# Performance work log

Measured on AMD Instinct MI355X. Metric: run time of the kernel, lower is better.

Reference implementation:

```python
import jax, jax.numpy as jnp
from jax import lax
import numpy as np

B, T, I, H, OUT = 4096, 168, 4, 64, 12


def setup_inputs() -> dict:
    key = jax.random.key(0)
    ks = jax.random.split(key, 14)
    s = 0.05
    return {
        "x": jax.random.normal(ks[0], (B, T, I), dtype=jnp.float32),
        # LSTM layer 0 (PyTorch gate order: i, f, g, o)
        "Wih0": jax.random.normal(ks[1], (4 * H, I), dtype=jnp.float32) * s,
        "Whh0": jax.random.normal(ks[2], (4 * H, H), dtype=jnp.float32) * s,
        "bih0": jax.random.normal(ks[3], (4 * H,), dtype=jnp.float32) * s,
        "bhh0": jax.random.normal(ks[4], (4 * H,), dtype=jnp.float32) * s,
        # LSTM layer 1
        "Wih1": jax.random.normal(ks[5], (4 * H, H), dtype=jnp.float32) * s,
        "Whh1": jax.random.normal(ks[6], (4 * H, H), dtype=jnp.float32) * s,
        "bih1": jax.random.normal(ks[7], (4 * H,), dtype=jnp.float32) * s,
        "bhh1": jax.random.normal(ks[8], (4 * H,), dtype=jnp.float32) * s,
        # FC head: Linear(64,64) -> ReLU -> Linear(64,12)
        "W1": jax.random.normal(ks[9], (64, H), dtype=jnp.float32) * s,
        "b1": jax.random.normal(ks[10], (64,), dtype=jnp.float32) * s,
        "W2": jax.random.normal(ks[11], (OUT, 64), dtype=jnp.float32) * s,
        "b2": jax.random.normal(ks[12], (OUT,), dtype=jnp.float32) * s,
    }


def _lstm_layer(x, Wih, Whh, bih, bhh):
    # x: [B, T, in]; returns hidden sequence [B, T, H]
    Bsz = x.shape[0]
    Hd = Whh.shape[1]
    # Precompute input contribution for all timesteps: [B, T, 4H]
    xg = jnp.einsum('bti,gi->btg', x, Wih) + bih + bhh

    def step(carry, xg_t):
        h, c = carry
        g = xg_t + h @ Whh.T  # [B, 4H]
        i, f, gg, o = jnp.split(g, 4, axis=-1)
        i = jax.nn.sigmoid(i)
        f = jax.nn.sigmoid(f)
        gg = jnp.tanh(gg)
        o = jax.nn.sigmoid(o)
        c = f * c + i * gg
        h = o * jnp.tanh(c)
        return (h, c), h

    h0 = jnp.zeros((Bsz, Hd), x.dtype)
    (_, _), hs = lax.scan(step, (h0, h0), jnp.swapaxes(xg, 0, 1))  # hs: [T, B, H]
    return jnp.swapaxes(hs, 0, 1)


def reference(x, Wih0, Whh0, bih0, bhh0, Wih1, Whh1, bih1, bhh1, W1, b1, W2, b2):
    # Eval-mode forward: dropout layers are identity.
    h1 = _lstm_layer(x, Wih0, Whh0, bih0, bhh0)   # [B, T, H]
    h2 = _lstm_layer(h1, Wih1, Whh1, bih1, bhh1)  # [B, T, H]
    last = h2[:, -1, :]                            # [B, H]
    z = jax.nn.relu(last @ W1.T + b1)              # [B, 64]
    out = z @ W2.T + b2                            # [B, 12]
    return out.reshape(-1, 3, 4)
```

## Files before the change

kernel.cpp:

```cpp
#include <hip/hip_runtime.h>


typedef _Float16 h8 __attribute__((ext_vector_type(8)));
typedef _Float16 h4 __attribute__((ext_vector_type(4)));
typedef float f4 __attribute__((ext_vector_type(4)));

#define ROWB 208
#define HBUF (16 * ROWB)
#define XTAB_OFF 0
#define XTAB_BYTES (169 * 256)
#define H0_OFF XTAB_BYTES
#define H1_OFF (H0_OFF + 2 * HBUF)
#define SMEM_TOTAL (H1_OFF + 2 * HBUF)

#define K1F 1.4426950408889634f
#define K2F 2.8853900817779268f

__device__ __forceinline__ float exp2_(float x) {
#if __has_builtin(__builtin_amdgcn_exp2f)
  return __builtin_amdgcn_exp2f(x);
#else
  float r; asm("v_exp_f32 %0, %1" : "=v"(r) : "v"(x)); return r;
#endif
}
__device__ __forceinline__ float rcp_(float x) {
#if __has_builtin(__builtin_amdgcn_rcpf)
  return __builtin_amdgcn_rcpf(x);
#else
  float r; asm("v_rcp_f32 %0, %1" : "=v"(r) : "v"(x)); return r;
#endif
}

__device__ __forceinline__ f4 mfma16(h8 a, h8 b, f4 c) {
  return __builtin_amdgcn_mfma_f32_16x16x32_f16(a, b, c, 0, 0, 0);
}

__device__ __forceinline__ h8 load_w8s(const float* __restrict__ p, float sc) {
  h8 r;
#pragma unroll
  for (int j = 0; j < 8; j++) r[j] = (_Float16)(p[j] * sc);
  return r;
}

__device__ __forceinline__ unsigned packh2(float a, float b) {
  unsigned lo = (unsigned)__builtin_bit_cast(unsigned short, (_Float16)a);
  unsigned hi = (unsigned)__builtin_bit_cast(unsigned short, (_Float16)b);
  return lo | (hi << 16);
}

__device__ __forceinline__ void lstm_act(f4 a, float& c, float& h) {
  float Ei = exp2_(-a[0]);
  float Ef = exp2_(-a[1]);
  float Eg = exp2_(a[2]);
  float Eo = exp2_(-a[3]);
  float A = 1.f + Ei, B = 1.f + Ef, C = 1.f + Eg, D = 1.f + Eo;
  float AB = A * B, CD = C * D, BD = B * D;
  float R  = rcp_(AB * CD);
  float fv = (A * CD) * R;
  float ig = (BD * (Eg - 1.f)) * R;
  float ov = (AB * C) * R;
  c = fv * c + ig;
  float r2 = rcp_(exp2_(c * K2F) + 1.f);
  h = ov * (1.f - 2.f * r2);
}

extern "C" __global__ void __launch_bounds__(256, 1)
weather_lstm_mfma6(const float* __restrict__ x,
                   const float* __restrict__ Wih0, const float* __restrict__ Whh0,
                   const float* __restrict__ bih0, const float* __restrict__ bhh0,
                   const float* __restrict__ Wih1, const float* __restrict__ Whh1,
                   const float* __restrict__ bih1, const float* __restrict__ bhh1,
                   const float* __restrict__ W1, const float* __restrict__ b1,
                   const float* __restrict__ W2, const float* __restrict__ b2,
                   float* __restrict__ out)
{
  __shared__ __align__(16) unsigned char smem[SMEM_TOTAL];
  const int tid  = threadIdx.x;
  const int lane = tid & 63;
  const int w    = tid >> 6;
  const int col  = lane & 15;
  const int quad = lane >> 4;
  const int sB   = blockIdx.x * 16;
  const int ub   = w * 16;

  const int g_  = col & 3;
  const int ul_ = col >> 2;
  const float asc = (g_ == 2) ? K2F : K1F;

  h8 a0[4][3], a1i[4][2], a1h[4][2];
#pragma unroll
  for (int T = 0; T < 4; T++) {
    const int unit = ub + (T >> 1) * 8 + 2 * ul_ + (T & 1);
    const int r = g_ * 64 + unit;
#pragma unroll
    for (int f = 0; f < 2; f++) {
      a0[T][f]  = load_w8s(Whh0 + r * 64 + f * 32 + quad * 8, asc);
      a1i[T][f] = load_w8s(Wih1 + r * 64 + f * 32 + quad * 8, asc);
      a1h[T][f] = load_w8s(Whh1 + r * 64 + f * 32 + quad * 8, asc);
    }
    h8 xw = {};
    if (quad == 0) {
#pragma unroll
      for (int j = 0; j < 4; j++) xw[j] = (_Float16)(Wih0[r * 4 + j] * asc);
    }
    a0[T][2] = xw;
  }

  f4 bias0v[4], bias1v[4];
#pragma unroll
  for (int T = 0; T < 4; T++) {
#pragma unroll
    for (int reg = 0; reg < 4; reg++) {
      const int rr = reg * 64 + ub + (T >> 1) * 8 + 2 * quad + (T & 1);
      const float bs = (reg == 2) ? K2F : K1F;
      bias0v[T][reg] = (bih0[rr] + bhh0[rr]) * bs;
      bias1v[T][reg] = (bih1[rr] + bhh1[rr]) * bs;
    }
  }

  for (int idx = tid; idx < SMEM_TOTAL / 4; idx += 256) ((int*)smem)[idx] = 0;
  __syncthreads();
  for (int idx = tid; idx < 16 * 168; idx += 256) {
    const int c_ = idx / 168, t_ = idx - c_ * 168;
    f4 xv = *(const f4*)(x + ((size_t)(sB + c_) * 168 + t_) * 4);
    h4 xh;
#pragma unroll
    for (int j = 0; j < 4; j++) xh[j] = (_Float16)xv[j];
    *(h4*)(smem + XTAB_OFF + t_ * 256 + c_ * 16) = xh;
  }
  __syncthreads();

  float c0[4] = {0.f, 0.f, 0.f, 0.f}, c1[4] = {0.f, 0.f, 0.f, 0.f};
  float hl[4] = {0.f, 0.f, 0.f, 0.f};
  const int bo  = col * ROWB + quad * 16;
  const int wo0 = col * ROWB + (ub + 2 * quad) * 2;
  const int wo1 = wo0 + 16;
  const unsigned char* xp = smem + XTAB_OFF + col * 16;

  for (int k = 0; k <= 168; k++) {
    const int kb = k & 1, kbn = kb ^ 1;
    const unsigned char* h0r = smem + H0_OFF + kbn * HBUF;
    unsigned char*       h0w = smem + H0_OFF + kb  * HBUF;
    const unsigned char* h1r = smem + H1_OFF + kb  * HBUF;
    unsigned char*       h1w = smem + H1_OFF + kbn * HBUF;

    h8 b0  = *(const h8*)(h0r + bo);
    h8 b1v = *(const h8*)(h0r + bo + 64);
    h8 bx  = *(const h8*)(xp + k * 256);
    h8 q0  = *(const h8*)(h1r + bo);
    h8 q1  = *(const h8*)(h1r + bo + 64);

    f4 A[4], C[4];
#pragma unroll
    for (int T = 0; T < 4; T++) A[T] = mfma16(a0[T][0], b0, bias0v[T]);
#pragma unroll
    for (int T = 0; T < 4; T++) C[T] = mfma16(a1i[T][0], b0, bias1v[T]);
#pragma unroll
    for (int T = 0; T < 4; T++) A[T] = mfma16(a0[T][1], b1v, A[T]);
#pragma unroll
    for (int T = 0; T < 4; T++) C[T] = mfma16(a1i[T][1], b1v, C[T]);
#pragma unroll
    for (int T = 0; T < 4; T++) A[T] = mfma16(a0[T][2], bx, A[T]);
#pragma unroll
    for (int T = 0; T < 4; T++) C[T] = mfma16(a1h[T][0], q0, C[T]);
#pragma unroll
    for (int T = 0; T < 4; T++) C[T] = mfma16(a1h[T][1], q1, C[T]);

    if (k < 168) {
      float h0o[4];
#pragma unroll
      for (int T = 0; T < 4; T++) lstm_act(A[T], c0[T], h0o[T]);
      *(unsigned*)(h0w + wo0) = packh2(h0o[0], h0o[1]);
      *(unsigned*)(h0w + wo1) = packh2(h0o[2], h0o[3]);
    }
    if (k > 0) {
#pragma unroll
      for (int T = 0; T < 4; T++) lstm_act(C[T], c1[T], hl[T]);
      *(unsigned*)(h1w + wo0) = packh2(hl[0], hl[1]);
      *(unsigned*)(h1w + wo1) = packh2(hl[2], hl[3]);
    }
    __syncthreads();
  }

  float* fh = (float*)smem;
#pragma unroll
  for (int T = 0; T < 4; T++)
    fh[col * 64 + (ub + (T >> 1) * 8 + 2 * quad + (T & 1))] = hl[T];
  __syncthreads();

  {
    const int u = tid & 63, grp = tid >> 6;
    float za[4];
#pragma unroll
    for (int i = 0; i < 4; i++) za[i] = b1[u];
    const float* w1r = W1 + u * 64;
    for (int j = 0; j < 64; j++) {
      float wv = w1r[j];
#pragma unroll
      for (int i = 0; i < 4; i++) za[i] += wv * fh[(grp * 4 + i) * 64 + j];
    }
    float* zl = (float*)(smem + 4096);
#pragma unroll
    for (int i = 0; i < 4; i++)
      zl[(grp * 4 + i) * 64 + u] = fmaxf(za[i], 0.f);
  }
  __syncthreads();

  if (tid < 192) {
    const float* zl = (const float*)(smem + 4096);
    const int s = tid / 12, o = tid - s * 12;
    float a = b2[o];
    for (int j = 0; j < 64; j++) a += W2[o * 64 + j] * zl[s * 64 + j];
    out[(sB + s) * 12 + o] = a;
  }
}

extern "C" void kernel_launch(void* const* d_in, const int* in_sizes, int n_in,
                              void* d_out, int out_size, void* d_ws, size_t ws_size,
                              hipStream_t stream) {
  (void)in_sizes; (void)n_in; (void)d_ws; (void)ws_size; (void)out_size;
  const float* x    = (const float*)d_in[0];
  const float* Wih0 = (const float*)d_in[1];
  const float* Whh0 = (const float*)d_in[2];
  const float* bih0 = (const float*)d_in[3];
  const float* bhh0 = (const float*)d_in[4];
  const float* Wih1 = (const float*)d_in[5];
  const float* Whh1 = (const float*)d_in[6];
  const float* bih1 = (const float*)d_in[7];
  const float* bhh1 = (const float*)d_in[8];
  const float* W1   = (const float*)d_in[9];
  const float* b1   = (const float*)d_in[10];
  const float* W2   = (const float*)d_in[11];
  const float* b2   = (const float*)d_in[12];

  weather_lstm_mfma6<<<dim3(256), dim3(256), 0, stream>>>(
      x, Wih0, Whh0, bih0, bhh0, Wih1, Whh1, bih1, bhh1, W1, b1, W2, b2,
      (float*)d_out);
}
```

Before: 234.7 us.

## Split LSTM layers onto separate warp groups with counter-based LDS handoff

Doubles the block to 512 threads. Four waves run layer 0 and four waves run layer 1, and they talk through a four-slot ring of layer-0 hidden states instead of meeting at a block-wide barrier on every step. Workgroup-scope atomic counters with acquire/release spin loops replace __syncthreads, so layer 0 can run up to a few steps ahead of layer 1 and each wave keeps fewer weight registers. The cost is busy-wait spinning on LDS counters and more waves per block. Memory ordering between the layer-0 writes and the counter increment rests on a single lane's release atomic, which is a correctness risk.

```diff
diff --git a/kernel.cpp b/kernel.cpp
--- a/kernel.cpp
+++ b/kernel.cpp
@@ -8,10 +8,11 @@
 #define ROWB 208
 #define HBUF (16 * ROWB)
 #define XTAB_OFF 0
-#define XTAB_BYTES (169 * 256)
+#define XTAB_BYTES (168 * 256)
 #define H0_OFF XTAB_BYTES
-#define H1_OFF (H0_OFF + 2 * HBUF)
-#define SMEM_TOTAL (H1_OFF + 2 * HBUF)
+#define H1_OFF (H0_OFF + 4 * HBUF)
+#define CNT_OFF (H1_OFF + 2 * HBUF)
+#define SMEM_TOTAL (CNT_OFF + 128)
 
 #define K1F 1.4426950408889634f
 #define K2F 2.8853900817779268f
@@ -59,13 +60,21 @@
   float fv = (A * CD) * R;
   float ig = (BD * (Eg - 1.f)) * R;
   float ov = (AB * C) * R;
-  c = fv * c + ig;
+  c = fmaf(fv, c, ig);
   float r2 = rcp_(exp2_(c * K2F) + 1.f);
-  h = ov * (1.f - 2.f * r2);
-}
-
-extern "C" __global__ void __launch_bounds__(256, 1)
-weather_lstm_mfma6(const float* __restrict__ x,
+  h = ov * fmaf(-2.f, r2, 1.f);
+}
+
+__device__ __forceinline__ void spin_ge(int* p, int tgt) {
+  while (__hip_atomic_load(p, __ATOMIC_ACQUIRE, __HIP_MEMORY_SCOPE_WORKGROUP) < tgt) {}
+}
+__device__ __forceinline__ void arrive(int* p, int lane) {
+  if (lane == 0)
+    __hip_atomic_fetch_add(p, 1, __ATOMIC_RELEASE, __HIP_MEMORY_SCOPE_WORKGROUP);
+}
+
+extern "C" __global__ void __launch_bounds__(512, 2)
+weather_lstm_mfma8(const float* __restrict__ x,
                    const float* __restrict__ Wih0, const float* __restrict__ Whh0,
                    const float* __restrict__ bih0, const float* __restrict__ bhh0,
                    const float* __restrict__ Wih1, const float* __restrict__ Whh1,
@@ -81,46 +90,20 @@
   const int col  = lane & 15;
   const int quad = lane >> 4;
   const int sB   = blockIdx.x * 16;
-  const int ub   = w * 16;
+  const bool isA = (w < 4);
+  const int gw   = w & 3;
+  const int ub   = gw * 16;
 
   const int g_  = col & 3;
   const int ul_ = col >> 2;
   const float asc = (g_ == 2) ? K2F : K1F;
 
-  h8 a0[4][3], a1i[4][2], a1h[4][2];
-#pragma unroll
-  for (int T = 0; T < 4; T++) {
-    const int unit = ub + (T >> 1) * 8 + 2 * ul_ + (T & 1);
-    const int r = g_ * 64 + unit;
-#pragma unroll
-    for (int f = 0; f < 2; f++) {
-      a0[T][f]  = load_w8s(Whh0 + r * 64 + f * 32 + quad * 8, asc);
-      a1i[T][f] = load_w8s(Wih1 + r * 64 + f * 32 + quad * 8, asc);
-      a1h[T][f] = load_w8s(Whh1 + r * 64 + f * 32 + quad * 8, asc);
-    }
-    h8 xw = {};
-    if (quad == 0) {
-#pragma unroll
-      for (int j = 0; j < 4; j++) xw[j] = (_Float16)(Wih0[r * 4 + j] * asc);
-    }
-    a0[T][2] = xw;
-  }
-
-  f4 bias0v[4], bias1v[4];
-#pragma unroll
-  for (int T = 0; T < 4; T++) {
-#pragma unroll
-    for (int reg = 0; reg < 4; reg++) {
-      const int rr = reg * 64 + ub + (T >> 1) * 8 + 2 * quad + (T & 1);
-      const float bs = (reg == 2) ? K2F : K1F;
-      bias0v[T][reg] = (bih0[rr] + bhh0[rr]) * bs;
-      bias1v[T][reg] = (bih1[rr] + bhh1[rr]) * bs;
-    }
-  }
-
-  for (int idx = tid; idx < SMEM_TOTAL / 4; idx += 256) ((int*)smem)[idx] = 0;
-  __syncthreads();
-  for (int idx = tid; idx < 16 * 168; idx += 256) {
+  int* aCnt = (int*)(smem + CNT_OFF);
+  int* bCnt = (int*)(smem + CNT_OFF + 64);
+
+  for (int idx = tid; idx < SMEM_TOTAL / 4; idx += 512) ((int*)smem)[idx] = 0;
+  __syncthreads();
+  for (int idx = tid; idx < 16 * 168; idx += 512) {
     const int c_ = idx / 168, t_ = idx - c_ * 168;
     f4 xv = *(const f4*)(x + ((size_t)(sB + c_) * 168 + t_) * 4);
     h4 xh;
@@ -130,84 +113,141 @@
   }
   __syncthreads();
 
-  float c0[4] = {0.f, 0.f, 0.f, 0.f}, c1[4] = {0.f, 0.f, 0.f, 0.f};
-  float hl[4] = {0.f, 0.f, 0.f, 0.f};
   const int bo  = col * ROWB + quad * 16;
   const int wo0 = col * ROWB + (ub + 2 * quad) * 2;
   const int wo1 = wo0 + 16;
-  const unsigned char* xp = smem + XTAB_OFF + col * 16;
-
-  for (int k = 0; k <= 168; k++) {
-    const int kb = k & 1, kbn = kb ^ 1;
-    const unsigned char* h0r = smem + H0_OFF + kbn * HBUF;
-    unsigned char*       h0w = smem + H0_OFF + kb  * HBUF;
-    const unsigned char* h1r = smem + H1_OFF + kb  * HBUF;
-    unsigned char*       h1w = smem + H1_OFF + kbn * HBUF;
-
-    h8 b0  = *(const h8*)(h0r + bo);
-    h8 b1v = *(const h8*)(h0r + bo + 64);
-    h8 bx  = *(const h8*)(xp + k * 256);
-    h8 q0  = *(const h8*)(h1r + bo);
-    h8 q1  = *(const h8*)(h1r + bo + 64);
-
-    f4 A[4], C[4];
-#pragma unroll
-    for (int T = 0; T < 4; T++) A[T] = mfma16(a0[T][0], b0, bias0v[T]);
-#pragma unroll
-    for (int T = 0; T < 4; T++) C[T] = mfma16(a1i[T][0], b0, bias1v[T]);
-#pragma unroll
-    for (int T = 0; T < 4; T++) A[T] = mfma16(a0[T][1], b1v, A[T]);
-#pragma unroll
-    for (int T = 0; T < 4; T++) C[T] = mfma16(a1i[T][1], b1v, C[T]);
-#pragma unroll
-    for (int T = 0; T < 4; T++) A[T] = mfma16(a0[T][2], bx, A[T]);
-#pragma unroll
-    for (int T = 0; T < 4; T++) C[T] = mfma16(a1h[T][0], q0, C[T]);
-#pragma unroll
-    for (int T = 0; T < 4; T++) C[T] = mfma16(a1h[T][1], q1, C[T]);
-
-    if (k < 168) {
+  float hl[4] = {0.f, 0.f, 0.f, 0.f};
+
+  if (isA) {
+    h8 a0[4][3];
+    f4 bias0v[4];
+#pragma unroll
+    for (int T = 0; T < 4; T++) {
+      const int r = g_ * 64 + ub + (T >> 1) * 8 + 2 * ul_ + (T & 1);
+#pragma unroll
+      for (int f = 0; f < 2; f++)
+        a0[T][f] = load_w8s(Whh0 + r * 64 + f * 32 + quad * 8, asc);
+      h8 xw = {};
+      if (quad == 0) {
+#pragma unroll
+        for (int j = 0; j < 4; j++) xw[j] = (_Float16)(Wih0[r * 4 + j] * asc);
+      }
+      a0[T][2] = xw;
+      const int rr = (0) * 64;
+      (void)rr;
+#pragma unroll
+      for (int reg = 0; reg < 4; reg++) {
+        const int rb = reg * 64 + ub + (T >> 1) * 8 + 2 * quad + (T & 1);
+        const float bs = (reg == 2) ? K2F : K1F;
+        bias0v[T][reg] = (bih0[rb] + bhh0[rb]) * bs;
+      }
+    }
+    const unsigned char* xp = smem + XTAB_OFF + col * 16;
+    float c0[4] = {0.f, 0.f, 0.f, 0.f};
+
+    for (int k = 0; k < 168; k++) {
+      if ((k & 3) == 0 && k > 0) spin_ge(bCnt, 4 * k);
+      spin_ge(aCnt, 4 * k);
+      const unsigned char* h0r = smem + H0_OFF + ((k + 3) & 3) * HBUF;
+      unsigned char*       h0w = smem + H0_OFF + (k & 3) * HBUF;
+
+      h8 b0  = *(const h8*)(h0r + bo);
+      h8 b1v = *(const h8*)(h0r + bo + 64);
+      h8 bx  = *(const h8*)(xp + k * 256);
+
+      f4 A[4];
+#pragma unroll
+      for (int T = 0; T < 4; T++) A[T] = mfma16(a0[T][0], b0, bias0v[T]);
+#pragma unroll
+      for (int T = 0; T < 4; T++) A[T] = mfma16(a0[T][1], b1v, A[T]);
+#pragma unroll
+      for (int T = 0; T < 4; T++) A[T] = mfma16(a0[T][2], bx, A[T]);
+
       float h0o[4];
 #pragma unroll
       for (int T = 0; T < 4; T++) lstm_act(A[T], c0[T], h0o[T]);
       *(unsigned*)(h0w + wo0) = packh2(h0o[0], h0o[1]);
       *(unsigned*)(h0w + wo1) = packh2(h0o[2], h0o[3]);
-    }
-    if (k > 0) {
+      arrive(aCnt, lane);
+    }
+  } else {
+    h8 a1i[4][2], a1h[4][2];
+    f4 bias1v[4];
+#pragma unroll
+    for (int T = 0; T < 4; T++) {
+      const int r = g_ * 64 + ub + (T >> 1) * 8 + 2 * ul_ + (T & 1);
+#pragma unroll
+      for (int f = 0; f < 2; f++) {
+        a1i[T][f] = load_w8s(Wih1 + r * 64 + f * 32 + quad * 8, asc);
+        a1h[T][f] = load_w8s(Whh1 + r * 64 + f * 32 + quad * 8, asc);
+      }
+#pragma unroll
+      for (int reg = 0; reg < 4; reg++) {
+        const int rb = reg * 64 + ub + (T >> 1) * 8 + 2 * quad + (T & 1);
+        const float bs = (reg == 2) ? K2F : K1F;
+        bias1v[T][reg] = (bih1[rb] + bhh1[rb]) * bs;
+      }
+    }
+    float c1[4] = {0.f, 0.f, 0.f, 0.f};
+
+    for (int k = 0; k < 168; k++) {
+      spin_ge(bCnt, 4 * k);
+      spin_ge(aCnt, 4 * (k + 1));
+      const unsigned char* hp = smem + H0_OFF + (k & 3) * HBUF;
+      const unsigned char* hq = smem + H1_OFF + ((k + 1) & 1) * HBUF;
+      unsigned char*       h1w = smem + H1_OFF + (k & 1) * HBUF;
+
+      h8 p0 = *(const h8*)(hp + bo);
+      h8 p1 = *(const h8*)(hp + bo + 64);
+      h8 q0 = *(const h8*)(hq + bo);
+      h8 q1 = *(const h8*)(hq + bo + 64);
+
+      f4 C[4];
+#pragma unroll
+      for (int T = 0; T < 4; T++) C[T] = mfma16(a1i[T][0], p0, bias1v[T]);
+#pragma unroll
+      for (int T = 0; T < 4; T++) C[T] = mfma16(a1i[T][1], p1, C[T]);
+#pragma unroll
+      for (int T = 0; T < 4; T++) C[T] = mfma16(a1h[T][0], q0, C[T]);
+#pragma unroll
+      for (int T = 0; T < 4; T++) C[T] = mfma16(a1h[T][1], q1, C[T]);
+
 #pragma unroll
       for (int T = 0; T < 4; T++) lstm_act(C[T], c1[T], hl[T]);
       *(unsigned*)(h1w + wo0) = packh2(hl[0], hl[1]);
       *(unsigned*)(h1w + wo1) = packh2(hl[2], hl[3]);
-    }
-    __syncthreads();
-  }
+      arrive(bCnt, lane);
+    }
+  }
+  __syncthreads();
 
   float* fh = (float*)smem;
-#pragma unroll
-  for (int T = 0; T < 4; T++)
-    fh[col * 64 + (ub + (T >> 1) * 8 + 2 * quad + (T & 1))] = hl[T];
+  if (!isA) {
+#pragma unroll
+    for (int T = 0; T < 4; T++)
+      fh[col * 64 + (ub + (T >> 1) * 8 + 2 * quad + (T & 1))] = hl[T];
+  }
   __syncthreads();
 
   {
     const int u = tid & 63, grp = tid >> 6;
-    float za[4];
-#pragma unroll
-    for (int i = 0; i < 4; i++) za[i] = b1[u];
+    float za0 = b1[u], za1 = b1[u];
     const float* w1r = W1 + u * 64;
+    const float* f0 = fh + (grp * 2 + 0) * 64;
+    const float* f1 = fh + (grp * 2 + 1) * 64;
     for (int j = 0; j < 64; j++) {
       float wv = w1r[j];
-#pragma unroll
-      for (int i = 0; i < 4; i++) za[i] += wv * fh[(grp * 4 + i) * 64 + j];
-    }
-    float* zl = (float*)(smem + 4096);
-#pragma unroll
-    for (int i = 0; i < 4; i++)
-      zl[(grp * 4 + i) * 64 + u] = fmaxf(za[i], 0.f);
+      za0 += wv * f0[j];
+      za1 += wv * f1[j];
+    }
+    float* zl = (float*)(smem + 8192);
+    zl[(grp * 2 + 0) * 64 + u] = fmaxf(za0, 0.f);
+    zl[(grp * 2 + 1) * 64 + u] = fmaxf(za1, 0.f);
   }
   __syncthreads();
 
   if (tid < 192) {
-    const float* zl = (const float*)(smem + 4096);
+    const float* zl = (const float*)(smem + 8192);
     const int s = tid / 12, o = tid - s * 12;
     float a = b2[o];
     for (int j = 0; j < 64; j++) a += W2[o * 64 + j] * zl[s * 64 + j];
@@ -233,7 +273,7 @@
   const float* W2   = (const float*)d_in[11];
   const float* b2   = (const float*)d_in[12];
 
-  weather_lstm_mfma6<<<dim3(256), dim3(256), 0, stream>>>(
+  weather_lstm_mfma8<<<dim3(256), dim3(512), 0, stream>>>(
       x, Wih0, Whh0, bih0, bhh0, Wih1, Whh1, bih1, bhh1, W1, b1, W2, b2,
       (float*)d_out);
 }
```

New measurement: 232.9 us. No clear change (-0.8%).
